# Performance work log

Measured on AMD Instinct MI355X. Metric: run time of the kernel, lower is better.

The kernel has to match this reference:

```python
import jax, jax.numpy as jnp
import numpy as np

N_DIM = 32
N_HEADS = 4
HEAD_SIZE = N_DIM // N_HEADS  # 8


def setup_inputs() -> dict:
    key = jax.random.key(0)
    ks = jax.random.split(key, 9)
    B, T = 16, 2048
    s = 1.0 / np.sqrt(N_DIM)
    inp = {
        "x": jax.random.normal(ks[0], (B, T, N_DIM), dtype=jnp.float32),
        "Wq": jax.random.uniform(ks[1], (N_DIM, N_DIM), jnp.float32, -s, s),
        "bq": jax.random.uniform(ks[2], (N_DIM,), jnp.float32, -s, s),
        "Wk": jax.random.uniform(ks[3], (N_DIM, N_DIM), jnp.float32, -s, s),
        "bk": jax.random.uniform(ks[4], (N_DIM,), jnp.float32, -s, s),
        "Wv": jax.random.uniform(ks[5], (N_DIM, N_DIM), jnp.float32, -s, s),
        "bv": jax.random.uniform(ks[6], (N_DIM,), jnp.float32, -s, s),
        "Wp": jax.random.uniform(ks[7], (N_DIM, N_DIM), jnp.float32, -s, s),
        "bp": jax.random.uniform(ks[8], (N_DIM,), jnp.float32, -s, s),
    }
    return inp


def reference(x, Wq, bq, Wk, bk, Wv, bv, Wp, bp):
    b, t, c = x.shape
    # nn.Linear: y = x @ W^T + b
    def heads(W, bias):
        y = jnp.einsum("btc,dc->btd", x, W) + bias
        return y.reshape(b, t, N_HEADS, HEAD_SIZE).transpose(0, 2, 1, 3)  # [b,h,t,d]

    q = heads(Wq, bq)
    k = heads(Wk, bk)
    v = heads(Wv, bv)

    scores = jnp.einsum("bhqd,bhkd->bhqk", q, k) / np.sqrt(HEAD_SIZE)  # [b,h,t,t]
    causal = jnp.tril(jnp.ones((t, t), dtype=bool))
    scores = jnp.where(causal[None, None], scores, -jnp.inf)
    weights = jax.nn.softmax(scores, axis=-1)
    # dropout layers are identity in eval mode
    z = jnp.einsum("bhqk,bhkd->bhqd", weights, v)
    z = z.transpose(0, 2, 1, 3).reshape(b, t, N_DIM)
    z = jnp.einsum("btc,dc->btd", z, Wp) + bp
    return z
```

## Files before the change

### kernel.cpp

```cpp
#include <hip/hip_runtime.h>
#include <math.h>

#define BB 16
#define TT 2048
#define CC 32
#define HH 4
#define DD 8

#define KBS 2056
#define VRS 264
#define VBS (9 * VRS)
#define ZP 33

typedef __fp16 h2  __attribute__((ext_vector_type(2)));
typedef __fp16 h8  __attribute__((ext_vector_type(8)));
typedef float  fx16 __attribute__((ext_vector_type(16)));
typedef int    i4v __attribute__((ext_vector_type(4)));

__device__ __forceinline__ h2 pkh(float a, float b) {
#if __has_builtin(__builtin_amdgcn_cvt_pkrtz)
    return __builtin_amdgcn_cvt_pkrtz(a, b);
#else
    h2 r; r.x = (__fp16)a; r.y = (__fp16)b; return r;
#endif
}

__device__ __forceinline__ float fexp2(float x) {
#if __has_builtin(__builtin_amdgcn_exp2f)
    return __builtin_amdgcn_exp2f(x);
#else
    return exp2f(x);
#endif
}

__device__ __forceinline__ int h2bits(h2 v) { return __builtin_bit_cast(int, v); }

__device__ __forceinline__ void makeP(const fx16& S, bool last, int thr, int hi, h8* P) {
    float pe[16];
    #pragma unroll
    for (int r = 0; r < 16; r++) {
        const int ko = (r & 3) + 8 * (r >> 2);
        float sv = S[r];
        if (last) sv = (ko <= thr) ? sv : -INFINITY;
        pe[r] = fexp2(sv);
    }
    int Hh[8];
    #pragma unroll
    for (int i = 0; i < 8; i++) Hh[i] = h2bits(pkh(pe[2*i], pe[2*i+1]));
    #pragma unroll
    for (int s = 0; s < 2; s++) {
        const int b0 = 4 * s;
        int own0 = hi ? Hh[b0+2] : Hh[b0+0];
        int own1 = hi ? Hh[b0+3] : Hh[b0+1];
        int snd0 = hi ? Hh[b0+0] : Hh[b0+2];
        int snd1 = hi ? Hh[b0+1] : Hh[b0+3];
        int rcv0 = __shfl_xor(snd0, 32);
        int rcv1 = __shfl_xor(snd1, 32);
        i4v f;
        f.x = hi ? rcv0 : own0;
        f.y = hi ? rcv1 : own1;
        f.z = hi ? own0 : rcv0;
        f.w = hi ? own1 : rcv1;
        P[s] = __builtin_bit_cast(h8, f);
    }
}

__global__ __launch_bounds__(256) void qkv_kernel(
    const float* __restrict__ x,
    const float* __restrict__ Wq, const float* __restrict__ bq,
    const float* __restrict__ Wk, const float* __restrict__ bk,
    const float* __restrict__ Wv, const float* __restrict__ bv,
    __fp16* __restrict__ Qo, __fp16* __restrict__ Ko, __fp16* __restrict__ Vo)
{
    __shared__ float Xs[256 * ZP];
    const int tid = threadIdx.x;
    const int m = blockIdx.y >> 2, h = blockIdx.y & 3;
    const int row0 = blockIdx.x * 256;

    {
        const float4* xg = (const float4*)(x + (size_t)row0 * CC);
        #pragma unroll
        for (int i = 0; i < 8; i++) {
            const int idx = tid + 256 * i;
            float4 f = xg[idx];
            const int w = idx * 4;
            float* d = &Xs[(w >> 5) * ZP + (w & 31)];
            d[0] = f.x; d[1] = f.y; d[2] = f.z; d[3] = f.w;
        }
    }
    __syncthreads();

    const int row = row0 + tid;
    const int b = row >> 11, t = row & 2047;
    const int bh = b * HH + h;

    float xr[CC];
    #pragma unroll
    for (int c = 0; c < CC; c++) xr[c] = Xs[tid * ZP + c];

    const float* W    = (m == 0) ? Wq : (m == 1) ? Wk : Wv;
    const float* bias = (m == 0) ? bq : (m == 1) ? bk : bv;

    float o[DD];
    #pragma unroll
    for (int d = 0; d < DD; d++) {
        const int dd = h * DD + d;
        float acc = bias[dd];
        #pragma unroll
        for (int c = 0; c < CC; c++) acc += xr[c] * W[dd * CC + c];
        o[d] = acc;
    }

    if (m == 0) {
        const float qs = 0.3535533905932738f * 1.4426950408889634f;
        i4v qw;
        qw.x = h2bits(pkh(o[0]*qs, o[1]*qs)); qw.y = h2bits(pkh(o[2]*qs, o[3]*qs));
        qw.z = h2bits(pkh(o[4]*qs, o[5]*qs)); qw.w = h2bits(pkh(o[6]*qs, o[7]*qs));
        *(i4v*)(Qo + ((size_t)bh * TT + t) * DD) = qw;
    } else if (m == 1) {
        i4v kw;
        kw.x = h2bits(pkh(o[0], o[1])); kw.y = h2bits(pkh(o[2], o[3]));
        kw.z = h2bits(pkh(o[4], o[5])); kw.w = h2bits(pkh(o[6], o[7]));
        *(i4v*)(Ko + ((size_t)bh * TT + t) * DD) = kw;
    } else {
        __fp16* vt = Vo + (size_t)bh * 9 * TT + t;
        #pragma unroll
        for (int d = 0; d < DD; d++) vt[d * TT] = (__fp16)o[d];
        vt[8 * TT] = (__fp16)1.0f;
    }
}

__global__ __launch_bounds__(512, 4) void attn_kernel(
    const __fp16* __restrict__ Qg, const __fp16* __restrict__ Kg,
    const __fp16* __restrict__ Vg,
    const float* __restrict__ Wp, const float* __restrict__ bp,
    float* __restrict__ out)
{
    __shared__ __align__(16) __fp16 KsS[8 * KBS];
    __shared__ __align__(16) __fp16 VtS[8 * VBS];
    __shared__ float zbuf[64 * ZP];

    const int tid  = threadIdx.x;
    const int b    = blockIdx.x & 15;
    const int ip   = blockIdx.x >> 4;
    const int w    = tid >> 6;
    const int h    = w & 3;
    const int qsel = w >> 2;
    const int lane = tid & 63;
    const int qc   = lane & 31;
    const int hi   = lane >> 5;

    const int bh  = b * HH + h;
    const int qb  = 32 * (qsel ? (63 - ip) : ip);
    const int keys_needed = qb + 32;
    const int nst = (keys_needed + 255) >> 8;

    h8 qf;
    {
        h8 qz;
        #pragma unroll
        for (int i = 0; i < 8; i++) qz[i] = (__fp16)0.0f;
        h8 qa = *(const h8*)(Qg + ((size_t)bh * TT + qb + qc) * DD);
        qf = hi ? qz : qa;
    }

    fx16 O, zc;
    #pragma unroll
    for (int i = 0; i < 16; i++) { O[i] = 0.0f; zc[i] = 0.0f; }

    const int vrow = (qc < 9) ? qc : 8;
    const int thr  = qc - 4 * hi;

    const __fp16* kgl = Kg + (size_t)bh * TT * DD;
    const __fp16* vgl = Vg + (size_t)bh * 9 * TT;
    __fp16* kld = KsS + w * KBS;
    __fp16* vld = VtS + w * VBS;
    const __fp16* kb = kld + qc * DD;
    const __fp16* vb = vld + vrow * VRS + 8 * hi;

    i4v kpre[4], vpre[5];
    {
        const i4v* ks = (const i4v*)kgl;
        #pragma unroll
        for (int r = 0; r < 4; r++) kpre[r] = ks[lane + 64 * r];
        #pragma unroll
        for (int r = 0; r < 5; r++) {
            int i = lane + 64 * r; if (i > 287) i = 287;
            vpre[r] = *(const i4v*)(vgl + (i >> 5) * TT + (i & 31) * 8);
        }
    }

    for (int sti = 0; sti < nst; sti++) {
        const int st = sti * 256;
        {
            i4v* kd = (i4v*)kld;
            #pragma unroll
            for (int r = 0; r < 4; r++) kd[lane + 64 * r] = kpre[r];
            #pragma unroll
            for (int r = 0; r < 5; r++) {
                const int i = lane + 64 * r;
                if (i < 288) *(i4v*)(vld + (i >> 5) * VRS + (i & 31) * 8) = vpre[r];
            }
        }
        if (sti + 1 < nst) {
            const int st2 = st + 256;
            const i4v* ks = (const i4v*)(kgl + (size_t)st2 * DD);
            #pragma unroll
            for (int r = 0; r < 4; r++) kpre[r] = ks[lane + 64 * r];
            #pragma unroll
            for (int r = 0; r < 5; r++) {
                int i = lane + 64 * r; if (i > 287) i = 287;
                vpre[r] = *(const i4v*)(vgl + (i >> 5) * TT + st2 + (i & 31) * 8);
            }
        }

        const int kend = min(st + 256, keys_needed);
        for (int kt = st; kt < kend; kt += 32) {
            h8 kf = *(const h8*)(kb + (kt - st) * DD);
            fx16 S = __builtin_amdgcn_mfma_f32_32x32x16_f16(kf, qf, zc, 0, 0, 0);
            h8 P[2];
            makeP(S, kt == qb, thr, hi, P);
            #pragma unroll
            for (int s = 0; s < 2; s++) {
                h8 vf = *(const h8*)(vb + (kt - st) + 16 * s);
                O = __builtin_amdgcn_mfma_f32_32x32x16_f16(vf, P[s], O, 0, 0, 0);
            }
        }
    }

    {
        const float inv = 1.0f / O[4];
        float* z = &zbuf[(qsel * 32 + qc) * ZP + h * DD + 4 * hi];
        z[0] = O[0]*inv; z[1] = O[1]*inv; z[2] = O[2]*inv; z[3] = O[3]*inv;
    }
    __syncthreads();

    {
        const int seg = tid >> 6;
        const int r = tid & 63;
        float zr[CC];
        #pragma unroll
        for (int c = 0; c < CC; c++) zr[c] = zbuf[r * ZP + c];
        float o[4];
        #pragma unroll
        for (int d = 0; d < 4; d++) {
            const int dd = seg * 4 + d;
            float acc = bp[dd];
            #pragma unroll
            for (int c = 0; c < CC; c++) acc += zr[c] * Wp[dd * CC + c];
            o[d] = acc;
        }
        const int qglob = (r < 32) ? (ip * 32 + r) : ((63 - ip) * 32 + (r - 32));
        float* dst = out + ((size_t)b * TT + qglob) * CC + seg * 4;
        *(float4*)dst = make_float4(o[0], o[1], o[2], o[3]);
    }
}

extern "C" void kernel_launch(void* const* d_in, const int* in_sizes, int n_in,
                              void* d_out, int out_size, void* d_ws, size_t ws_size,
                              hipStream_t stream) {
    const float* x  = (const float*)d_in[0];
    const float* Wq = (const float*)d_in[1];
    const float* bq = (const float*)d_in[2];
    const float* Wk = (const float*)d_in[3];
    const float* bk = (const float*)d_in[4];
    const float* Wv = (const float*)d_in[5];
    const float* bv = (const float*)d_in[6];
    const float* Wp = (const float*)d_in[7];
    const float* bp = (const float*)d_in[8];
    float* out = (float*)d_out;

    const size_t NE = (size_t)BB * HH * TT * DD;
    __fp16* Qh = (__fp16*)d_ws;
    __fp16* Kh = Qh + NE;
    __fp16* Vt = Kh + NE;

    qkv_kernel<<<dim3(BB * TT / 256, 12), 256, 0, stream>>>(x, Wq, bq, Wk, bk, Wv, bv, Qh, Kh, Vt);
    attn_kernel<<<dim3(BB * 32), 512, 0, stream>>>(Qh, Kh, Vt, Wp, bp, out);
}
```

Baseline: 127.3 us.

## Share K/V LDS tiles across query waves, fuse QKV per head, use permlane32 swap

The attention kernel now has only the four high-query waves (qsel) stage K/V into shared memory per head. The low-query waves reuse those tiles, which halves LDS footprint and global K/V loads. The cost is two block-wide barriers per stage, and the low waves sit idle until the high waves finish their longer key range. The QKV kernel computes Q, K and V for one head in a single block so the x tile is loaded once instead of three times. The P-fragment exchange uses permlane32_swap in place of two shuffles when that builtin is available.

```diff
diff --git a/kernel.cpp b/kernel.cpp
--- a/kernel.cpp
+++ b/kernel.cpp
@@ -16,6 +16,7 @@
 typedef __fp16 h8  __attribute__((ext_vector_type(8)));
 typedef float  fx16 __attribute__((ext_vector_type(16)));
 typedef int    i4v __attribute__((ext_vector_type(4)));
+typedef int    i2v __attribute__((ext_vector_type(2)));
 
 __device__ __forceinline__ h2 pkh(float a, float b) {
 #if __has_builtin(__builtin_amdgcn_cvt_pkrtz)
@@ -47,6 +48,19 @@
     int Hh[8];
     #pragma unroll
     for (int i = 0; i < 8; i++) Hh[i] = h2bits(pkh(pe[2*i], pe[2*i+1]));
+#if __has_builtin(__builtin_amdgcn_permlane32_swap)
+    #pragma unroll
+    for (int s = 0; s < 2; s++) {
+        const int b0 = 4 * s;
+        auto ra = __builtin_amdgcn_permlane32_swap(Hh[b0+0], Hh[b0+2], false, false);
+        auto rb = __builtin_amdgcn_permlane32_swap(Hh[b0+1], Hh[b0+3], false, false);
+        i2v pa = __builtin_bit_cast(i2v, ra);
+        i2v pb = __builtin_bit_cast(i2v, rb);
+        i4v f;
+        f.x = pa.x; f.y = pb.x; f.z = pa.y; f.w = pb.y;
+        P[s] = __builtin_bit_cast(h8, f);
+    }
+#else
     #pragma unroll
     for (int s = 0; s < 2; s++) {
         const int b0 = 4 * s;
@@ -63,6 +77,7 @@
         f.w = hi ? own1 : rcv1;
         P[s] = __builtin_bit_cast(h8, f);
     }
+#endif
 }
 
 __global__ __launch_bounds__(256) void qkv_kernel(
@@ -74,7 +89,7 @@
 {
     __shared__ float Xs[256 * ZP];
     const int tid = threadIdx.x;
-    const int m = blockIdx.y >> 2, h = blockIdx.y & 3;
+    const int h = blockIdx.y;
     const int row0 = blockIdx.x * 256;
 
     {
@@ -98,31 +113,47 @@
     #pragma unroll
     for (int c = 0; c < CC; c++) xr[c] = Xs[tid * ZP + c];
 
-    const float* W    = (m == 0) ? Wq : (m == 1) ? Wk : Wv;
-    const float* bias = (m == 0) ? bq : (m == 1) ? bk : bv;
-
-    float o[DD];
-    #pragma unroll
-    for (int d = 0; d < DD; d++) {
-        const int dd = h * DD + d;
-        float acc = bias[dd];
-        #pragma unroll
-        for (int c = 0; c < CC; c++) acc += xr[c] * W[dd * CC + c];
-        o[d] = acc;
-    }
-
-    if (m == 0) {
+    {
+        float o[DD];
+        #pragma unroll
+        for (int d = 0; d < DD; d++) {
+            const int dd = h * DD + d;
+            float acc = bq[dd];
+            #pragma unroll
+            for (int c = 0; c < CC; c++) acc += xr[c] * Wq[dd * CC + c];
+            o[d] = acc;
+        }
         const float qs = 0.3535533905932738f * 1.4426950408889634f;
         i4v qw;
         qw.x = h2bits(pkh(o[0]*qs, o[1]*qs)); qw.y = h2bits(pkh(o[2]*qs, o[3]*qs));
         qw.z = h2bits(pkh(o[4]*qs, o[5]*qs)); qw.w = h2bits(pkh(o[6]*qs, o[7]*qs));
         *(i4v*)(Qo + ((size_t)bh * TT + t) * DD) = qw;
-    } else if (m == 1) {
+    }
+    {
+        float o[DD];
+        #pragma unroll
+        for (int d = 0; d < DD; d++) {
+            const int dd = h * DD + d;
+            float acc = bk[dd];
+            #pragma unroll
+            for (int c = 0; c < CC; c++) acc += xr[c] * Wk[dd * CC + c];
+            o[d] = acc;
+        }
         i4v kw;
         kw.x = h2bits(pkh(o[0], o[1])); kw.y = h2bits(pkh(o[2], o[3]));
         kw.z = h2bits(pkh(o[4], o[5])); kw.w = h2bits(pkh(o[6], o[7]));
         *(i4v*)(Ko + ((size_t)bh * TT + t) * DD) = kw;
-    } else {
+    }
+    {
+        float o[DD];
+        #pragma unroll
+        for (int d = 0; d < DD; d++) {
+            const int dd = h * DD + d;
+            float acc = bv[dd];
+            #pragma unroll
+            for (int c = 0; c < CC; c++) acc += xr[c] * Wv[dd * CC + c];
+            o[d] = acc;
+        }
         __fp16* vt = Vo + (size_t)bh * 9 * TT + t;
         #pragma unroll
         for (int d = 0; d < DD; d++) vt[d * TT] = (__fp16)o[d];
@@ -136,8 +167,8 @@
     const float* __restrict__ Wp, const float* __restrict__ bp,
     float* __restrict__ out)
 {
-    __shared__ __align__(16) __fp16 KsS[8 * KBS];
-    __shared__ __align__(16) __fp16 VtS[8 * VBS];
+    __shared__ __align__(16) __fp16 KsS[4 * KBS];
+    __shared__ __align__(16) __fp16 VtS[4 * VBS];
     __shared__ float zbuf[64 * ZP];
 
     const int tid  = threadIdx.x;
@@ -153,7 +184,7 @@
     const int bh  = b * HH + h;
     const int qb  = 32 * (qsel ? (63 - ip) : ip);
     const int keys_needed = qb + 32;
-    const int nst = (keys_needed + 255) >> 8;
+    const int nstBlk = (32 * (63 - ip) + 32 + 255) >> 8;
 
     h8 qf;
     {
@@ -173,13 +204,13 @@
 
     const __fp16* kgl = Kg + (size_t)bh * TT * DD;
     const __fp16* vgl = Vg + (size_t)bh * 9 * TT;
-    __fp16* kld = KsS + w * KBS;
-    __fp16* vld = VtS + w * VBS;
+    __fp16* kld = KsS + h * KBS;
+    __fp16* vld = VtS + h * VBS;
     const __fp16* kb = kld + qc * DD;
     const __fp16* vb = vld + vrow * VRS + 8 * hi;
 
     i4v kpre[4], vpre[5];
-    {
+    if (qsel) {
         const i4v* ks = (const i4v*)kgl;
         #pragma unroll
         for (int r = 0; r < 4; r++) kpre[r] = ks[lane + 64 * r];
@@ -190,9 +221,9 @@
         }
     }
 
-    for (int sti = 0; sti < nst; sti++) {
+    for (int sti = 0; sti < nstBlk; sti++) {
         const int st = sti * 256;
-        {
+        if (qsel) {
             i4v* kd = (i4v*)kld;
             #pragma unroll
             for (int r = 0; r < 4; r++) kd[lane + 64 * r] = kpre[r];
@@ -201,18 +232,19 @@
                 const int i = lane + 64 * r;
                 if (i < 288) *(i4v*)(vld + (i >> 5) * VRS + (i & 31) * 8) = vpre[r];
             }
-        }
-        if (sti + 1 < nst) {
-            const int st2 = st + 256;
-            const i4v* ks = (const i4v*)(kgl + (size_t)st2 * DD);
-            #pragma unroll
-            for (int r = 0; r < 4; r++) kpre[r] = ks[lane + 64 * r];
-            #pragma unroll
-            for (int r = 0; r < 5; r++) {
-                int i = lane + 64 * r; if (i > 287) i = 287;
-                vpre[r] = *(const i4v*)(vgl + (i >> 5) * TT + st2 + (i & 31) * 8);
+            if (sti + 1 < nstBlk) {
+                const int st2 = st + 256;
+                const i4v* ks = (const i4v*)(kgl + (size_t)st2 * DD);
+                #pragma unroll
+                for (int r = 0; r < 4; r++) kpre[r] = ks[lane + 64 * r];
+                #pragma unroll
+                for (int r = 0; r < 5; r++) {
+                    int i = lane + 64 * r; if (i > 287) i = 287;
+                    vpre[r] = *(const i4v*)(vgl + (i >> 5) * TT + st2 + (i & 31) * 8);
+                }
             }
         }
+        __syncthreads();
 
         const int kend = min(st + 256, keys_needed);
         for (int kt = st; kt < kend; kt += 32) {
@@ -226,6 +258,7 @@
                 O = __builtin_amdgcn_mfma_f32_32x32x16_f16(vf, P[s], O, 0, 0, 0);
             }
         }
+        __syncthreads();
     }
 
     {
@@ -275,6 +308,6 @@
     __fp16* Kh = Qh + NE;
     __fp16* Vt = Kh + NE;
 
-    qkv_kernel<<<dim3(BB * TT / 256, 12), 256, 0, stream>>>(x, Wq, bq, Wk, bk, Wv, bv, Qh, Kh, Vt);
+    qkv_kernel<<<dim3(BB * TT / 256, HH), 256, 0, stream>>>(x, Wq, bq, Wk, bk, Wv, bv, Qh, Kh, Vt);
     attn_kernel<<<dim3(BB * 32), 512, 0, stream>>>(Qh, Kh, Vt, Wp, bp, out);
 }
```

Result: faster. 112.9 us (-11.3%).
